# Kernel tuning notes

Measured on AMD Instinct MI355X. Metric: run time of the kernel, lower is better.

The kernel has to match this reference:

```python
import jax, jax.numpy as jnp
import numpy as np

N_NODES = 50000
N_EDGES = 800000
D = 128
SAME_W = 0.3
CROSS_W = 1.0


def setup_inputs() -> dict:
    key = jax.random.key(0)
    k1, k2, k3, k4, k5 = jax.random.split(key, 5)
    x = jax.random.normal(k1, (N_NODES, D), dtype=jnp.float32)
    edge_index = jax.random.randint(k2, (2, N_EDGES), 0, N_NODES, dtype=jnp.int64)
    edge_weight = jax.random.uniform(k3, (N_EDGES,), dtype=jnp.float32)
    Wr1 = jax.random.normal(k4, (D, D), dtype=jnp.float32) * (1.0 / np.sqrt(D))
    Wr2 = jax.random.normal(k5, (D, D), dtype=jnp.float32) * (1.0 / np.sqrt(D))
    return {"x": x, "edge_index": edge_index, "edge_weight": edge_weight,
            "Wr1": Wr1, "Wr2": Wr2, "cell_len": 20000}


def _node_types(idx, cell_len):
    # get_node_types: type 0 if idx <= cell_len, else 1 (note the <=, faithful to source)
    return (idx > cell_len).astype(jnp.int32)


def _conv_layer(x, src, dst, per_edge_w, Wr, n_nodes):
    # gather -> weight -> scatter-mean -> + root linear
    msg = x[src] * per_edge_w[:, None]                       # [E, D]
    agg = jax.ops.segment_sum(msg, dst, num_segments=n_nodes)  # [N, D]
    cnt = jax.ops.segment_sum(jnp.ones_like(per_edge_w), dst, num_segments=n_nodes)
    agg = agg / jnp.maximum(cnt, 1.0)[:, None]               # mean aggr (0 if no edges)
    return agg + x @ Wr.T                                     # lin_r, bias=False


def reference(x, edge_index, edge_weight, Wr1, Wr2, cell_len):
    src, dst = edge_index[0], edge_index[1]
    same = _node_types(src, cell_len) == _node_types(dst, cell_len)
    type_w = jnp.where(same, SAME_W, CROSS_W).astype(x.dtype)
    w = type_w * edge_weight                                  # [E]
    n_nodes = x.shape[0]
    h = _conv_layer(x, src, dst, w, Wr1, n_nodes)
    out = _conv_layer(h, src, dst, w, Wr2, n_nodes)
    return out
```

## Files before the change

kernel.cpp:

```cpp
#include <hip/hip_runtime.h>
#include <cstdint>
#include <cstddef>

#define D 128
#define SAME_W 0.3f
#define CROSS_W 1.0f
#define NSLICE 8
#define EPT 8
#define CAP 64
#define RT 2

using bf16x8 = __attribute__((ext_vector_type(8))) __bf16;
using f32x4  = __attribute__((ext_vector_type(4))) float;

__device__ __forceinline__ unsigned bf16rne(float f) {
    unsigned u = __float_as_uint(f);
    return (u + 0x7FFFu + ((u >> 16) & 1u)) >> 16;
}

__global__ __launch_bounds__(256) void k_fill_capped(const int* __restrict__ src,
                                                     const int* __restrict__ dst,
                                                     const float* __restrict__ ew,
                                                     const int* __restrict__ cell_len,
                                                     int* __restrict__ cnt,
                                                     unsigned* __restrict__ meta,
                                                     int E, int sliceLen) {
    const int slice = blockIdx.x & (NSLICE - 1);
    const int lo = slice * sliceLen, hi = lo + sliceLen;
    const int base = (blockIdx.x >> 3) * (256 * EPT) + threadIdx.x;
    const int c = *cell_len;
    #pragma unroll
    for (int u = 0; u < EPT; ++u) {
        int e = base + u * 256;
        if (e < E) {
            int d = dst[e];
            if (d >= lo && d < hi) {
                int s = src[e];
                float wt = ew[e] * (((s > c) == (d > c)) ? SAME_W : CROSS_W);
                int pos = atomicAdd(&cnt[d], 1);
                if (pos < CAP)
                    meta[d * CAP + pos] = (unsigned)s | (bf16rne(wt) << 16);
            }
        }
    }
}

__global__ __launch_bounds__(256) void k_split4(const float4* __restrict__ in,
                                                uint2* __restrict__ oh,
                                                uint2* __restrict__ ol, int nvec) {
    int i = blockIdx.x * blockDim.x + threadIdx.x;
    if (i >= nvec) return;
    float4 v = in[i];
    unsigned h0 = bf16rne(v.x), h1 = bf16rne(v.y), h2 = bf16rne(v.z), h3 = bf16rne(v.w);
    uint2 rh;
    rh.x = h0 | (h1 << 16);
    rh.y = h2 | (h3 << 16);
    oh[i] = rh;
    float r0 = v.x - __uint_as_float(h0 << 16);
    float r1 = v.y - __uint_as_float(h1 << 16);
    float r2 = v.z - __uint_as_float(h2 << 16);
    float r3 = v.w - __uint_as_float(h3 << 16);
    uint2 rl;
    rl.x = bf16rne(r0) | (bf16rne(r1) << 16);
    rl.y = bf16rne(r2) | (bf16rne(r3) << 16);
    ol[i] = rl;
}

__global__ __launch_bounds__(256) void k_wcombine(const float* __restrict__ W1,
                                                  const float* __restrict__ W2,
                                                  unsigned* __restrict__ wsh,
                                                  unsigned* __restrict__ w12h,
                                                  unsigned* __restrict__ w12l) {
    int t = blockIdx.x * 256 + threadIdx.x;
    int j = t >> 6, kp = t & 63;
    int k0 = kp * 2;
    float d0 = 0.f, d1 = 0.f;
    #pragma unroll 4
    for (int m = 0; m < D; ++m) {
        float a = W2[j * D + m];
        d0 = fmaf(a, W1[m * D + k0], d0);
        d1 = fmaf(a, W1[m * D + k0 + 1], d1);
    }
    float s0 = W1[j * D + k0] + W2[j * D + k0];
    float s1 = W1[j * D + k0 + 1] + W2[j * D + k0 + 1];
    wsh[j * 64 + kp] = bf16rne(s0) | (bf16rne(s1) << 16);
    unsigned h0 = bf16rne(d0), h1 = bf16rne(d1);
    w12h[j * 64 + kp] = h0 | (h1 << 16);
    float r0 = d0 - __uint_as_float(h0 << 16);
    float r1 = d1 - __uint_as_float(h1 << 16);
    w12l[j * 64 + kp] = bf16rne(r0) | (bf16rne(r1) << 16);
}

template <bool OUT_BF16>
__global__ __launch_bounds__(256) void k_agg_cap(const unsigned* __restrict__ xin,
                                                 const unsigned* __restrict__ meta,
                                                 const int* __restrict__ cnt,
                                                 void* __restrict__ outp, int N) {
    int gid = blockIdx.x * blockDim.x + threadIdx.x;
    int node = gid >> 6;
    int lane = gid & 63;
    if (node >= N) return;
    const int cn = cnt[node];
    const int start = node * CAP;
    const int end = start + min(cn, CAP);
    float ax0 = 0.f, ay0 = 0.f, ax1 = 0.f, ay1 = 0.f;
    int i = start;
    #pragma unroll 1
    for (; i + 8 <= end; i += 8) {
        unsigned m[8];
        #pragma unroll
        for (int u = 0; u < 8; ++u) m[u] = meta[i + u];
        unsigned v[8];
        #pragma unroll
        for (int u = 0; u < 8; ++u) v[u] = xin[(size_t)(m[u] & 0xFFFFu) * 64 + lane];
        #pragma unroll
        for (int u = 0; u < 8; ++u) {
            float wt = __uint_as_float(m[u] & 0xFFFF0000u);
            float vx = __uint_as_float(v[u] << 16);
            float vy = __uint_as_float(v[u] & 0xFFFF0000u);
            if (u & 1) { ax1 = fmaf(vx, wt, ax1); ay1 = fmaf(vy, wt, ay1); }
            else       { ax0 = fmaf(vx, wt, ax0); ay0 = fmaf(vy, wt, ay0); }
        }
    }
    for (; i < end; ++i) {
        unsigned m = meta[i];
        float wt = __uint_as_float(m & 0xFFFF0000u);
        unsigned v = xin[(size_t)(m & 0xFFFFu) * 64 + lane];
        ax0 = fmaf(__uint_as_float(v << 16), wt, ax0);
        ay0 = fmaf(__uint_as_float(v & 0xFFFF0000u), wt, ay0);
    }
    const float scale = 1.0f / (float)max(cn, 1);
    const float rx = (ax0 + ax1) * scale, ry = (ay0 + ay1) * scale;
    if (OUT_BF16) {
        ((unsigned*)outp)[(size_t)node * 64 + lane] = bf16rne(rx) | (bf16rne(ry) << 16);
    } else {
        ((float2*)outp)[(size_t)node * 64 + lane] = make_float2(rx, ry);
    }
}

__global__ __launch_bounds__(256, 1) void k_gemm2(
    const uint4* __restrict__ xh4, const uint4* __restrict__ xl4,
    const uint4* __restrict__ a1h4,
    const uint4* __restrict__ w12h4, const uint4* __restrict__ w12l4,
    const uint4* __restrict__ wsh4,
    const float* __restrict__ cin,
    float* __restrict__ fout, int N)
{
    const int t = threadIdx.x;
    const int wave = t >> 6, lane = t & 63;
    const int n0 = blockIdx.x * (RT * 16);
    const int j0 = wave * 32;
    const int lr = lane & 15;
    const int q  = lane >> 4;

    union FU { uint4 u; bf16x8 v; };

    FU wA[2][4], wB[2][4], wC[2][4];
    #pragma unroll
    for (int jt = 0; jt < 2; ++jt) {
        const int brow = (j0 + jt * 16 + lr) * 16 + q;
        #pragma unroll
        for (int ks = 0; ks < 4; ++ks) {
            wA[jt][ks].u = w12h4[brow + ks * 4];
            wB[jt][ks].u = w12l4[brow + ks * 4];
            wC[jt][ks].u = wsh4[brow + ks * 4];
        }
    }

    FU axh[RT][4], axl[RT][4], aa1[RT][4];
    #pragma unroll
    for (int at = 0; at < RT; ++at) {
        int row = n0 + at * 16 + lr;
        if (row > N - 1) row = N - 1;
        const int arow = row * 16 + q;
        #pragma unroll
        for (int ks = 0; ks < 4; ++ks) {
            axh[at][ks].u = xh4[arow + ks * 4];
            axl[at][ks].u = xl4[arow + ks * 4];
            aa1[at][ks].u = a1h4[arow + ks * 4];
        }
    }

    float ci[RT][2][4];
    #pragma unroll
    for (int at = 0; at < RT; ++at)
        #pragma unroll
        for (int jt = 0; jt < 2; ++jt)
            #pragma unroll
            for (int r = 0; r < 4; ++r) {
                int rr = n0 + at * 16 + q * 4 + r;
                if (rr > N - 1) rr = N - 1;
                ci[at][jt][r] = cin[(size_t)rr * D + j0 + jt * 16 + lr];
            }

    f32x4 c[RT][2];
    #pragma unroll
    for (int at = 0; at < RT; ++at)
        #pragma unroll
        for (int jt = 0; jt < 2; ++jt)
            c[at][jt] = (f32x4){0.f, 0.f, 0.f, 0.f};

    #pragma unroll
    for (int at = 0; at < RT; ++at)
        #pragma unroll
        for (int jt = 0; jt < 2; ++jt)
            #pragma unroll
            for (int ks = 0; ks < 4; ++ks) {
                c[at][jt] = __builtin_amdgcn_mfma_f32_16x16x32_bf16(axh[at][ks].v, wA[jt][ks].v, c[at][jt], 0, 0, 0);
                c[at][jt] = __builtin_amdgcn_mfma_f32_16x16x32_bf16(axl[at][ks].v, wA[jt][ks].v, c[at][jt], 0, 0, 0);
                c[at][jt] = __builtin_amdgcn_mfma_f32_16x16x32_bf16(axh[at][ks].v, wB[jt][ks].v, c[at][jt], 0, 0, 0);
                c[at][jt] = __builtin_amdgcn_mfma_f32_16x16x32_bf16(aa1[at][ks].v, wC[jt][ks].v, c[at][jt], 0, 0, 0);
            }

    #pragma unroll
    for (int at = 0; at < RT; ++at)
        #pragma unroll
        for (int jt = 0; jt < 2; ++jt)
            #pragma unroll
            for (int r = 0; r < 4; ++r) {
                int rr = n0 + at * 16 + q * 4 + r;
                if (rr < N)
                    fout[(size_t)rr * D + j0 + jt * 16 + lr] = c[at][jt][r] + ci[at][jt][r];
            }
}

extern "C" void kernel_launch(void* const* d_in, const int* in_sizes, int n_in,
                              void* d_out, int out_size, void* d_ws, size_t ws_size,
                              hipStream_t stream) {
    const float* x        = (const float*)d_in[0];
    const int*   ei       = (const int*)d_in[1];
    const float* ew       = (const float*)d_in[2];
    const float* Wr1      = (const float*)d_in[3];
    const float* Wr2      = (const float*)d_in[4];
    const int*   cell_len = (const int*)d_in[5];

    const int N = in_sizes[0] / D;
    const int E = in_sizes[1] / 2;
    const int* src = ei;
    const int* dst = ei + E;

    char* ws = (char*)d_ws;
    size_t off = 0;
    unsigned* meta = (unsigned*)(ws + off); off += (size_t)4 * CAP * N;
    int*      cnt  = (int*)     (ws + off); off += (size_t)4 * N;
    off = (off + 255) & ~(size_t)255;
    unsigned* xh   = (unsigned*)(ws + off); off += (size_t)2 * N * D;
    unsigned* xl   = (unsigned*)(ws + off); off += (size_t)2 * N * D;
    unsigned* a1h  = (unsigned*)(ws + off); off += (size_t)2 * N * D;
    float*    a2   = (float*)   (ws + off); off += (size_t)4 * N * D;
    unsigned* wsh  = (unsigned*)(ws + off); off += (size_t)2 * D * D;
    unsigned* w12h = (unsigned*)(ws + off); off += (size_t)2 * D * D;
    unsigned* w12l = (unsigned*)(ws + off); off += (size_t)2 * D * D;
    if (ws_size < off) return;
    float* out = (float*)d_out;

    hipMemsetAsync(cnt, 0, (size_t)4 * N, stream);

    const int sliceLen = (N + NSLICE - 1) / NSLICE;
    const int edgeBlocks = ((E + 256 * EPT - 1) / (256 * EPT)) * NSLICE;
    const int aggBlocks = (N + 3) / 4;
    const int gemmBlocks = (N + RT * 16 - 1) / (RT * 16);
    const int xvec = N * D / 4;

    k_fill_capped<<<edgeBlocks, 256, 0, stream>>>(src, dst, ew, cell_len,
                                                  cnt, meta, E, sliceLen);
    k_split4<<<(xvec + 255) / 256, 256, 0, stream>>>((const float4*)x,
                                                     (uint2*)xh, (uint2*)xl, xvec);
    k_wcombine<<<32, 256, 0, stream>>>(Wr1, Wr2, wsh, w12h, w12l);

    k_agg_cap<true ><<<aggBlocks, 256, 0, stream>>>(xh,  meta, cnt, (void*)a1h, N);
    k_agg_cap<false><<<aggBlocks, 256, 0, stream>>>(a1h, meta, cnt, (void*)a2,  N);

    k_gemm2<<<gemmBlocks, 256, 0, stream>>>((const uint4*)xh, (const uint4*)xl,
                                            (const uint4*)a1h,
                                            (const uint4*)w12h, (const uint4*)w12l,
                                            (const uint4*)wsh, a2, out, N);
}
```

Baseline: 255.5 us.

## Vectorize meta loads, store second aggregate as bf16, persistent double-buffered GEMM

The aggregation kernel now reads edge metadata as uint4 with a 16-wide unrolled gather. It also always emits bf16, so the second aggregate is half the size. The GEMM becomes persistent, running 512 blocks over 16-row tiles with register double buffering that loads the next tile while the current one computes, and its occupancy hint is raised to 2. The aim is to cut memory traffic and hide load latency. In exchange, rounding the second aggregate to bf16 adds precision loss.

Measured after the change: 232.5 us. 1.1x faster.

```diff
diff --git a/kernel.cpp b/kernel.cpp
--- a/kernel.cpp
+++ b/kernel.cpp
@@ -8,7 +8,7 @@
 #define NSLICE 8
 #define EPT 8
 #define CAP 64
-#define RT 2
+#define GEMM_BLOCKS 512
 
 using bf16x8 = __attribute__((ext_vector_type(8))) __bf16;
 using f32x4  = __attribute__((ext_vector_type(4))) float;
@@ -91,64 +91,79 @@
     w12l[j * 64 + kp] = bf16rne(r0) | (bf16rne(r1) << 16);
 }
 
-template <bool OUT_BF16>
 __global__ __launch_bounds__(256) void k_agg_cap(const unsigned* __restrict__ xin,
-                                                 const unsigned* __restrict__ meta,
+                                                 const uint4* __restrict__ meta4,
                                                  const int* __restrict__ cnt,
-                                                 void* __restrict__ outp, int N) {
+                                                 unsigned* __restrict__ outp, int N) {
     int gid = blockIdx.x * blockDim.x + threadIdx.x;
     int node = gid >> 6;
     int lane = gid & 63;
     if (node >= N) return;
-    const int cn = cnt[node];
-    const int start = node * CAP;
-    const int end = start + min(cn, CAP);
+    const int cn0 = cnt[node];
+    const int cn = min(cn0, CAP);
+    const uint4* mrow = meta4 + (size_t)node * (CAP / 4);
     float ax0 = 0.f, ay0 = 0.f, ax1 = 0.f, ay1 = 0.f;
-    int i = start;
+    int i = 0;
     #pragma unroll 1
-    for (; i + 8 <= end; i += 8) {
-        unsigned m[8];
-        #pragma unroll
-        for (int u = 0; u < 8; ++u) m[u] = meta[i + u];
-        unsigned v[8];
-        #pragma unroll
-        for (int u = 0; u < 8; ++u) v[u] = xin[(size_t)(m[u] & 0xFFFFu) * 64 + lane];
-        #pragma unroll
-        for (int u = 0; u < 8; ++u) {
-            float wt = __uint_as_float(m[u] & 0xFFFF0000u);
+    for (; i + 16 <= cn; i += 16) {
+        uint4 mq[4];
+        #pragma unroll
+        for (int u = 0; u < 4; ++u) mq[u] = mrow[(i >> 2) + u];
+        unsigned v[16];
+        #pragma unroll
+        for (int u = 0; u < 16; ++u) {
+            unsigned m = ((const unsigned*)mq)[u];
+            v[u] = xin[(size_t)(m & 0xFFFFu) * 64 + lane];
+        }
+        #pragma unroll
+        for (int u = 0; u < 16; ++u) {
+            unsigned m = ((const unsigned*)mq)[u];
+            float wt = __uint_as_float(m & 0xFFFF0000u);
             float vx = __uint_as_float(v[u] << 16);
             float vy = __uint_as_float(v[u] & 0xFFFF0000u);
             if (u & 1) { ax1 = fmaf(vx, wt, ax1); ay1 = fmaf(vy, wt, ay1); }
             else       { ax0 = fmaf(vx, wt, ax0); ay0 = fmaf(vy, wt, ay0); }
         }
     }
-    for (; i < end; ++i) {
-        unsigned m = meta[i];
+    #pragma unroll 1
+    for (; i + 4 <= cn; i += 4) {
+        uint4 mq = mrow[i >> 2];
+        unsigned v[4];
+        #pragma unroll
+        for (int u = 0; u < 4; ++u)
+            v[u] = xin[(size_t)(((const unsigned*)&mq)[u] & 0xFFFFu) * 64 + lane];
+        #pragma unroll
+        for (int u = 0; u < 4; ++u) {
+            unsigned m = ((const unsigned*)&mq)[u];
+            float wt = __uint_as_float(m & 0xFFFF0000u);
+            float vx = __uint_as_float(v[u] << 16);
+            float vy = __uint_as_float(v[u] & 0xFFFF0000u);
+            if (u & 1) { ax1 = fmaf(vx, wt, ax1); ay1 = fmaf(vy, wt, ay1); }
+            else       { ax0 = fmaf(vx, wt, ax0); ay0 = fmaf(vy, wt, ay0); }
+        }
+    }
+    for (; i < cn; ++i) {
+        unsigned m = ((const unsigned*)mrow)[i];
         float wt = __uint_as_float(m & 0xFFFF0000u);
         unsigned v = xin[(size_t)(m & 0xFFFFu) * 64 + lane];
         ax0 = fmaf(__uint_as_float(v << 16), wt, ax0);
         ay0 = fmaf(__uint_as_float(v & 0xFFFF0000u), wt, ay0);
     }
-    const float scale = 1.0f / (float)max(cn, 1);
+    const float scale = 1.0f / (float)max(cn0, 1);
     const float rx = (ax0 + ax1) * scale, ry = (ay0 + ay1) * scale;
-    if (OUT_BF16) {
-        ((unsigned*)outp)[(size_t)node * 64 + lane] = bf16rne(rx) | (bf16rne(ry) << 16);
-    } else {
-        ((float2*)outp)[(size_t)node * 64 + lane] = make_float2(rx, ry);
-    }
-}
-
-__global__ __launch_bounds__(256, 1) void k_gemm2(
+    outp[(size_t)node * 64 + lane] = bf16rne(rx) | (bf16rne(ry) << 16);
+}
+
+__global__ __launch_bounds__(256, 2) void k_gemm2(
     const uint4* __restrict__ xh4, const uint4* __restrict__ xl4,
     const uint4* __restrict__ a1h4,
     const uint4* __restrict__ w12h4, const uint4* __restrict__ w12l4,
     const uint4* __restrict__ wsh4,
-    const float* __restrict__ cin,
-    float* __restrict__ fout, int N)
+    const unsigned* __restrict__ a2b,
+    float* __restrict__ fout, int N, int nTiles)
 {
     const int t = threadIdx.x;
     const int wave = t >> 6, lane = t & 63;
-    const int n0 = blockIdx.x * (RT * 16);
     const int j0 = wave * 32;
     const int lr = lane & 15;
     const int q  = lane >> 4;
@@ -167,61 +182,71 @@
         }
     }
 
-    FU axh[RT][4], axl[RT][4], aa1[RT][4];
-    #pragma unroll
-    for (int at = 0; at < RT; ++at) {
-        int row = n0 + at * 16 + lr;
-        if (row > N - 1) row = N - 1;
-        const int arow = row * 16 + q;
-        #pragma unroll
-        for (int ks = 0; ks < 4; ++ks) {
-            axh[at][ks].u = xh4[arow + ks * 4];
-            axl[at][ks].u = xl4[arow + ks * 4];
-            aa1[at][ks].u = a1h4[arow + ks * 4];
-        }
-    }
-
-    float ci[RT][2][4];
-    #pragma unroll
-    for (int at = 0; at < RT; ++at)
-        #pragma unroll
-        for (int jt = 0; jt < 2; ++jt)
-            #pragma unroll
-            for (int r = 0; r < 4; ++r) {
-                int rr = n0 + at * 16 + q * 4 + r;
-                if (rr > N - 1) rr = N - 1;
-                ci[at][jt][r] = cin[(size_t)rr * D + j0 + jt * 16 + lr];
-            }
-
-    f32x4 c[RT][2];
-    #pragma unroll
-    for (int at = 0; at < RT; ++at)
-        #pragma unroll
-        for (int jt = 0; jt < 2; ++jt)
-            c[at][jt] = (f32x4){0.f, 0.f, 0.f, 0.f};
-
-    #pragma unroll
-    for (int at = 0; at < RT; ++at)
-        #pragma unroll
-        for (int jt = 0; jt < 2; ++jt)
-            #pragma unroll
-            for (int ks = 0; ks < 4; ++ks) {
-                c[at][jt] = __builtin_amdgcn_mfma_f32_16x16x32_bf16(axh[at][ks].v, wA[jt][ks].v, c[at][jt], 0, 0, 0);
-                c[at][jt] = __builtin_amdgcn_mfma_f32_16x16x32_bf16(axl[at][ks].v, wA[jt][ks].v, c[at][jt], 0, 0, 0);
-                c[at][jt] = __builtin_amdgcn_mfma_f32_16x16x32_bf16(axh[at][ks].v, wB[jt][ks].v, c[at][jt], 0, 0, 0);
-                c[at][jt] = __builtin_amdgcn_mfma_f32_16x16x32_bf16(aa1[at][ks].v, wC[jt][ks].v, c[at][jt], 0, 0, 0);
-            }
-
-    #pragma unroll
-    for (int at = 0; at < RT; ++at)
-        #pragma unroll
-        for (int jt = 0; jt < 2; ++jt)
-            #pragma unroll
-            for (int r = 0; r < 4; ++r) {
-                int rr = n0 + at * 16 + q * 4 + r;
-                if (rr < N)
-                    fout[(size_t)rr * D + j0 + jt * 16 + lr] = c[at][jt][r] + ci[at][jt][r];
-            }
+#define LOAD_TILE(BX, BL, BA, BC, TILE) do {                                   \
+    int row_ = (TILE) * 16 + lr; if (row_ > N - 1) row_ = N - 1;               \
+    const int ar_ = row_ * 16 + q;                                             \
+    _Pragma("unroll")                                                          \
+    for (int ks = 0; ks < 4; ++ks) {                                           \
+        BX[ks].u = xh4[ar_ + ks * 4];                                          \
+        BL[ks].u = xl4[ar_ + ks * 4];                                          \
+        BA[ks].u = a1h4[ar_ + ks * 4];                                         \
+    }                                                                          \
+    _Pragma("unroll")                                                          \
+    for (int jt = 0; jt < 2; ++jt)                                             \
+        _Pragma("unroll")                                                      \
+        for (int r = 0; r < 4; ++r) {                                          \
+            int rr_ = (TILE) * 16 + q * 4 + r; if (rr_ > N - 1) rr_ = N - 1;   \
+            BC[jt * 4 + r] = a2b[(size_t)rr_ * 64 + ((j0 + jt * 16 + lr) >> 1)]; \
+        }                                                                      \
+} while (0)
+
+#define COMPUTE_STORE(BX, BL, BA, BC, TILE) do {                               \
+    f32x4 c_[2];                                                               \
+    c_[0] = (f32x4){0.f, 0.f, 0.f, 0.f};                                       \
+    c_[1] = (f32x4){0.f, 0.f, 0.f, 0.f};                                       \
+    _Pragma("unroll")                                                          \
+    for (int jt = 0; jt < 2; ++jt)                                             \
+        _Pragma("unroll")                                                      \
+        for (int ks = 0; ks < 4; ++ks) {                                       \
+            c_[jt] = __builtin_amdgcn_mfma_f32_16x16x32_bf16(BX[ks].v, wA[jt][ks].v, c_[jt], 0, 0, 0); \
+            c_[jt] = __builtin_amdgcn_mfma_f32_16x16x32_bf16(BL[ks].v, wA[jt][ks].v, c_[jt], 0, 0, 0); \
+            c_[jt] = __builtin_amdgcn_mfma_f32_16x16x32_bf16(BX[ks].v, wB[jt][ks].v, c_[jt], 0, 0, 0); \
+            c_[jt] = __builtin_amdgcn_mfma_f32_16x16x32_bf16(BA[ks].v, wC[jt][ks].v, c_[jt], 0, 0, 0); \
+        }                                                                      \
+    _Pragma("unroll")                                                          \
+    for (int jt = 0; jt < 2; ++jt)                                             \
+        _Pragma("unroll")                                                      \
+        for (int r = 0; r < 4; ++r) {                                          \
+            int rr_ = (TILE) * 16 + q * 4 + r;                                 \
+            if (rr_ < N) {                                                     \
+                unsigned w_ = BC[jt * 4 + r];                                  \
+                float ci_ = __uint_as_float((lr & 1) ? (w_ & 0xFFFF0000u) : (w_ << 16)); \
+                fout[(size_t)rr_ * D + j0 + jt * 16 + lr] = c_[jt][r] + ci_;   \
+            }                                                                  \
+        }                                                                      \
+} while (0)
+
+    FU Axh[4], Axl[4], Aa1[4]; unsigned Aci[8];
+    FU Bxh[4], Bxl[4], Ba1[4]; unsigned Bci[8];
+
+    int tile = blockIdx.x;
+    const int step = gridDim.x;
+    if (tile >= nTiles) return;
+    LOAD_TILE(Axh, Axl, Aa1, Aci, tile);
+    while (true) {
+        int tn = tile + step;
+        if (tn < nTiles) LOAD_TILE(Bxh, Bxl, Ba1, Bci, tn);
+        COMPUTE_STORE(Axh, Axl, Aa1, Aci, tile);
+        tile = tn;
+        if (tile >= nTiles) break;
+        tn = tile + step;
+        if (tn < nTiles) LOAD_TILE(Axh, Axl, Aa1, Aci, tn);
+        COMPUTE_STORE(Bxh, Bxl, Ba1, Bci, tile);
+        tile = tn;
+        if (tile >= nTiles) break;
+    }
+#undef LOAD_TILE
+#undef COMPUTE_STORE
 }
 
 extern "C" void kernel_launch(void* const* d_in, const int* in_sizes, int n_in,
@@ -247,7 +272,7 @@
     unsigned* xh   = (unsigned*)(ws + off); off += (size_t)2 * N * D;
     unsigned* xl   = (unsigned*)(ws + off); off += (size_t)2 * N * D;
     unsigned* a1h  = (unsigned*)(ws + off); off += (size_t)2 * N * D;
-    float*    a2   = (float*)   (ws + off); off += (size_t)4 * N * D;
+    unsigned* a2b  = (unsigned*)(ws + off); off += (size_t)2 * N * D;
     unsigned* wsh  = (unsigned*)(ws + off); off += (size_t)2 * D * D;
     unsigned* w12h = (unsigned*)(ws + off); off += (size_t)2 * D * D;
     unsigned* w12l = (unsigned*)(ws + off); off += (size_t)2 * D * D;
@@ -259,7 +284,7 @@
     const int sliceLen = (N + NSLICE - 1) / NSLICE;
     const int edgeBlocks = ((E + 256 * EPT - 1) / (256 * EPT)) * NSLICE;
     const int aggBlocks = (N + 3) / 4;
-    const int gemmBlocks = (N + RT * 16 - 1) / (RT * 16);
+    const int nTiles = (N + 15) / 16;
     const int xvec = N * D / 4;
 
     k_fill_capped<<<edgeBlocks, 256, 0, stream>>>(src, dst, ew, cell_len,
@@ -268,11 +293,11 @@
                                                      (uint2*)xh, (uint2*)xl, xvec);
     k_wcombine<<<32, 256, 0, stream>>>(Wr1, Wr2, wsh, w12h, w12l);
 
-    k_agg_cap<true ><<<aggBlocks, 256, 0, stream>>>(xh,  meta, cnt, (void*)a1h, N);
-    k_agg_cap<false><<<aggBlocks, 256, 0, stream>>>(a1h, meta, cnt, (void*)a2,  N);
-
-    k_gemm2<<<gemmBlocks, 256, 0, stream>>>((const uint4*)xh, (const uint4*)xl,
-                                            (const uint4*)a1h,
-                                            (const uint4*)w12h, (const uint4*)w12l,
-                                            (const uint4*)wsh, a2, out, N);
-}
+    k_agg_cap<<<aggBlocks, 256, 0, stream>>>(xh, (const uint4*)meta, cnt, a1h, N);
+    k_agg_cap<<<aggBlocks, 256, 0, stream>>>(a1h, (const uint4*)meta, cnt, a2b, N);
+
+    k_gemm2<<<GEMM_BLOCKS, 256, 0, stream>>>((const uint4*)xh, (const uint4*)xl,
+                                             (const uint4*)a1h,
+                                             (const uint4*)w12h, (const uint4*)w12l,
+                                             (const uint4*)wsh, a2b, out, N, nTiles);
+}
```
